# Kernel optimization log

Measured on AMD Instinct MI355X. Metric: run time of the kernel, lower is better.

Reference implementation:

```python
import jax, jax.numpy as jnp
import numpy as np

D = 20                 # input_dim
N = 1_000_000          # batch
NC = 2 ** (D + 1)      # number of dummy expert Linear(1,1) modules


def setup_inputs() -> dict:
    key = jax.random.key(0)
    ks = jax.random.split(key, 12)
    x = jax.random.randint(ks[0], (N, D), 0, 2).astype(jnp.float32)   # binary features
    t = jax.random.randint(ks[1], (N, 1), 0, 2).astype(jnp.float32)   # binary treatment
    y = jax.random.normal(ks[2], (N, 1), dtype=jnp.float32)           # outcome fed to dummy linears
    # Encoder dummy experts: one (w, b) pair per combination of (t, x)
    qz_w = jax.random.normal(ks[3], (NC,), dtype=jnp.float32) * 0.1
    qz_b = jax.random.normal(ks[4], (NC,), dtype=jnp.float32) * 0.1
    # Decoder per-feature Linear(1,1) for binary x
    dx_w = jax.random.normal(ks[5], (D,), dtype=jnp.float32) * 0.1
    dx_b = jax.random.normal(ks[6], (D,), dtype=jnp.float32) * 0.1
    # Decoder scalar Linear(1,1) heads
    t_w = jax.random.normal(ks[7], (), dtype=jnp.float32) * 0.1
    t_b = jnp.zeros((), jnp.float32)
    y0_w = jax.random.normal(ks[8], (), dtype=jnp.float32) * 0.1
    y0_b = jnp.zeros((), jnp.float32)
    y1_w = jax.random.normal(ks[9], (), dtype=jnp.float32) * 0.1
    y1_b = jnp.zeros((), jnp.float32)
    pz_logit = jnp.zeros((1,), jnp.float32)
    return {"x": x, "t": t, "y": y, "qz_w": qz_w, "qz_b": qz_b,
            "dx_w": dx_w, "dx_b": dx_b, "t_w": t_w, "t_b": t_b,
            "y0_w": y0_w, "y0_b": y0_b, "y1_w": y1_w, "y1_b": y1_b,
            "pz_logit": pz_logit}


def _combo_index(x, t):
    # itertools.product([0,1], repeat=D+1): combs[i][0] is the t bit (MSB),
    # combs[i][1:] are the x bits, so i = t*2^D + sum_j x_j * 2^(D-1-j).
    pow2 = (2 ** jnp.arange(D - 1, -1, -1)).astype(jnp.int32)   # [D]
    return t[:, 0].astype(jnp.int32) * (2 ** D) + x.astype(jnp.int32) @ pow2  # [N]


def _decode(z, t, dx_w, dx_b, t_w, t_b, y0_w, y0_b, y1_w, y1_b):
    # Vectorized form of per-feature Linear(1,1) loops: x_logits[:, i] = w_i*z + b_i
    x_logits = z * dx_w[None, :] + dx_b[None, :]          # [N, D]
    t_logits = z * t_w + t_b                              # [N, 1]
    y_logits = (z * y1_w + y1_b) * t + (z * y0_w + y0_b) * (1.0 - t)  # [N, 1]
    return x_logits, t_logits, y_logits


def reference(x, t, y, qz_w, qz_b, dx_w, dx_b, t_w, t_b,
              y0_w, y0_b, y1_w, y1_b, pz_logit):
    # Encoder (z_mode='binary'): sum over all 2^(D+1) experts of
    # (w_i*y + b_i) * onehot_mask_i == gather by combination index (inputs binary).
    idx = _combo_index(x, t)                                  # [N]
    z_logits = (qz_w[idx] * y[:, 0] + qz_b[idx])[:, None]     # [N, 1]
    n = x.shape[0]
    z0 = jnp.zeros((n, 1), jnp.float32)
    z1 = jnp.ones((n, 1), jnp.float32)
    x_logits0, t_logits0, y_logits0 = _decode(z0, t, dx_w, dx_b, t_w, t_b, y0_w, y0_b, y1_w, y1_b)
    x_logits1, t_logits1, y_logits1 = _decode(z1, t, dx_w, dx_b, t_w, t_b, y0_w, y0_b, y1_w, y1_b)
    return (z_logits, x_logits0, x_logits1, t_logits0, t_logits1,
            y_logits0, y_logits1, pz_logit)
```

## Files before the change

kernel.cpp:

```cpp
#include <hip/hip_runtime.h>

constexpr int D = 20;

typedef float f4 __attribute__((ext_vector_type(4)));
typedef unsigned int u32;

__device__ __forceinline__ u32 bf16_rne(float f) {
    u32 u = __float_as_uint(f);
    return (u + 0x7FFFu + ((u >> 16) & 1u)) >> 16;
}

__global__ __launch_bounds__(256) void cevae_build_tab(
    const f4* __restrict__ qw, const f4* __restrict__ qb,
    uint4* __restrict__ tab, int nq)
{
    int i = blockIdx.x * 256 + threadIdx.x;
    if (i >= nq) return;
    f4 w = qw[i];
    f4 b = qb[i];
    uint4 o;
    o.x = (bf16_rne(w.x) << 16) | bf16_rne(b.x);
    o.y = (bf16_rne(w.y) << 16) | bf16_rne(b.y);
    o.z = (bf16_rne(w.z) << 16) | bf16_rne(b.z);
    o.w = (bf16_rne(w.w) << 16) | bf16_rne(b.w);
    tab[i] = o;
}

__device__ __forceinline__ u32 combo_idx(const f4* xr, float tv) {
    f4 a = xr[0], b = xr[1], c = xr[2], d = xr[3], e = xr[4];
    u32 id = (tv != 0.0f) ? (1u << 20) : 0u;
    id |= ((u32)a.x) << 19; id |= ((u32)a.y) << 18;
    id |= ((u32)a.z) << 17; id |= ((u32)a.w) << 16;
    id |= ((u32)b.x) << 15; id |= ((u32)b.y) << 14;
    id |= ((u32)b.z) << 13; id |= ((u32)b.w) << 12;
    id |= ((u32)c.x) << 11; id |= ((u32)c.y) << 10;
    id |= ((u32)c.z) << 9;  id |= ((u32)c.w) << 8;
    id |= ((u32)d.x) << 7;  id |= ((u32)d.y) << 6;
    id |= ((u32)d.z) << 5;  id |= ((u32)d.w) << 4;
    id |= ((u32)e.x) << 3;  id |= ((u32)e.y) << 2;
    id |= ((u32)e.z) << 1;  id |= ((u32)e.w);
    return id;
}

template <bool USE_TAB>
__global__ __launch_bounds__(256) void cevae_fused8_kernel(
    const float* __restrict__ x, const float* __restrict__ t,
    const float* __restrict__ y, const u32* __restrict__ tab,
    const float* __restrict__ qz_w, const float* __restrict__ qz_b,
    const float* __restrict__ dx_w, const float* __restrict__ dx_b,
    const float* __restrict__ sc_tw, const float* __restrict__ sc_tb,
    const float* __restrict__ sc_y0w, const float* __restrict__ sc_y0b,
    const float* __restrict__ sc_y1w, const float* __restrict__ sc_y1b,
    const float* __restrict__ pz, float* __restrict__ out, int n_rows,
    int n_fill_blocks)
{
    int bid = blockIdx.x;
    int g = bid >> 3;
    size_t o3 = (size_t)n_rows * (size_t)(1 + 2 * D);

    if ((g & 3) == 0) {
        int sub = (g >> 2) * 8 + (bid & 7);
        int Qr = n_rows >> 2;
        int m = sub * 256 + threadIdx.x;
        if (m >= Qr) return;

        int n0 = m, n1 = m + Qr, n2 = m + 2 * Qr, n3 = m + 3 * Qr;

        float t0 = t[n0], t1 = t[n1], t2 = t[n2], t3 = t[n3];
        u32 i0 = combo_idx((const f4*)(x + (size_t)n0 * D), t0);
        u32 i1 = combo_idx((const f4*)(x + (size_t)n1 * D), t1);
        u32 i2 = combo_idx((const f4*)(x + (size_t)n2 * D), t2);
        u32 i3 = combo_idx((const f4*)(x + (size_t)n3 * D), t3);

        float y0v = y[n0], y1v = y[n1], y2v = y[n2], y3v = y[n3];

        float z0, z1, z2, z3;
        if (USE_TAB) {
            u32 g0 = tab[i0], g1 = tab[i1], g2 = tab[i2], g3 = tab[i3];
            z0 = fmaf(__uint_as_float(g0 & 0xFFFF0000u), y0v, __uint_as_float(g0 << 16));
            z1 = fmaf(__uint_as_float(g1 & 0xFFFF0000u), y1v, __uint_as_float(g1 << 16));
            z2 = fmaf(__uint_as_float(g2 & 0xFFFF0000u), y2v, __uint_as_float(g2 << 16));
            z3 = fmaf(__uint_as_float(g3 & 0xFFFF0000u), y3v, __uint_as_float(g3 << 16));
        } else {
            z0 = fmaf(qz_w[i0], y0v, qz_b[i0]);
            z1 = fmaf(qz_w[i1], y1v, qz_b[i1]);
            z2 = fmaf(qz_w[i2], y2v, qz_b[i2]);
            z3 = fmaf(qz_w[i3], y3v, qz_b[i3]);
        }
        out[n0] = z0;
        out[n1] = z1;
        out[n2] = z2;
        out[n3] = z3;

        float y0w = *sc_y0w, y0b = *sc_y0b;
        float y1w = *sc_y1w, y1b = *sc_y1b;
        float dy0 = y1b - y0b;
        float dy1 = (y1w + y1b) - (y0w + y0b), c1 = y0w + y0b;

        float* yl0 = out + o3 + 2 * (size_t)n_rows;
        float* yl1 = out + o3 + 3 * (size_t)n_rows;
        yl0[n0] = fmaf(t0, dy0, y0b);
        yl0[n1] = fmaf(t1, dy0, y0b);
        yl0[n2] = fmaf(t2, dy0, y0b);
        yl0[n3] = fmaf(t3, dy0, y0b);
        yl1[n0] = fmaf(t0, dy1, c1);
        yl1[n1] = fmaf(t1, dy1, c1);
        yl1[n2] = fmaf(t2, dy1, c1);
        yl1[n3] = fmaf(t3, dy1, c1);
        if (m == 0) out[o3 + 4 * (size_t)n_rows] = pz[0];
    } else {
        int fsub = (g - (g >> 2) - 1) * 8 + (bid & 7);
        unsigned Q = (unsigned)n_rows * D / 4;
        f4* r0 = (f4*)(out + n_rows);
        f4* r1 = r0 + Q;
        unsigned stride = (unsigned)n_fill_blocks * 256;
        unsigned q0 = (unsigned)fsub * 256 + threadIdx.x;
        for (unsigned q = q0; q < Q; q += stride) {
            int cb = (int)(q % 5u) * 4;
            float b0 = dx_b[cb + 0], b1 = dx_b[cb + 1];
            float b2 = dx_b[cb + 2], b3 = dx_b[cb + 3];
            float w0 = dx_w[cb + 0], w1 = dx_w[cb + 1];
            float w2 = dx_w[cb + 2], w3 = dx_w[cb + 3];
            f4 v0 = {b0, b1, b2, b3};
            f4 v1 = {w0 + b0, w1 + b1, w2 + b2, w3 + b3};
            __builtin_nontemporal_store(v0, r0 + q);
            __builtin_nontemporal_store(v1, r1 + q);
        }
        float tw = *sc_tw, tb = *sc_tb;
        f4 s0 = {tb, tb, tb, tb};
        float t1v = tw + tb;
        f4 s1 = {t1v, t1v, t1v, t1v};
        unsigned Qt = (unsigned)n_rows / 4;
        f4* h0 = (f4*)(out + o3);
        f4* h1 = (f4*)(out + o3 + (size_t)n_rows);
        for (unsigned q = q0; q < Qt; q += stride) {
            __builtin_nontemporal_store(s0, h0 + q);
            __builtin_nontemporal_store(s1, h1 + q);
        }
    }
}

extern "C" void kernel_launch(void* const* d_in, const int* in_sizes, int n_in,
                              void* d_out, int out_size, void* d_ws, size_t ws_size,
                              hipStream_t stream) {
    const float* x    = (const float*)d_in[0];
    const float* t    = (const float*)d_in[1];
    const float* y    = (const float*)d_in[2];
    const float* qz_w = (const float*)d_in[3];
    const float* qz_b = (const float*)d_in[4];
    const float* dx_w = (const float*)d_in[5];
    const float* dx_b = (const float*)d_in[6];
    const float* t_w  = (const float*)d_in[7];
    const float* t_b  = (const float*)d_in[8];
    const float* y0_w = (const float*)d_in[9];
    const float* y0_b = (const float*)d_in[10];
    const float* y1_w = (const float*)d_in[11];
    const float* y1_b = (const float*)d_in[12];
    const float* pz   = (const float*)d_in[13];
    float* out = (float*)d_out;

    int n_rows = in_sizes[0] / D;
    int nc     = in_sizes[3];

    int Qr = n_rows / 4;
    int n_rows_blocks = (Qr + 255) / 256;
    int n_rows_groups = (n_rows_blocks + 7) / 8;
    int n_groups = n_rows_groups * 4;
    int n_fill_blocks = (n_groups - n_rows_groups) * 8;

    size_t tab_bytes = (size_t)nc * sizeof(u32);
    if (ws_size >= tab_bytes) {
        uint4* tab = (uint4*)d_ws;
        int nq = nc / 4;
        cevae_build_tab<<<(nq + 255) / 256, 256, 0, stream>>>(
            (const f4*)qz_w, (const f4*)qz_b, tab, nq);
        cevae_fused8_kernel<true><<<n_groups * 8, 256, 0, stream>>>(
            x, t, y, (const u32*)tab, qz_w, qz_b, dx_w, dx_b, t_w, t_b,
            y0_w, y0_b, y1_w, y1_b, pz, out, n_rows, n_fill_blocks);
    } else {
        cevae_fused8_kernel<false><<<n_groups * 8, 256, 0, stream>>>(
            x, t, y, nullptr, qz_w, qz_b, dx_w, dx_b, t_w, t_b,
            y0_w, y0_b, y1_w, y1_b, pz, out, n_rows, n_fill_blocks);
    }
}
```

Before: 81.32 us.

## Fuse table build with constant fill and split row gather into separate kernel

The bf16 table build now shares one launch with the constant x/t logit fill, and the per-row gather (z, y logits) moves into its own kernel that runs afterwards. Before, the table build ran alone and the gather and fill blocks were interleaved in one launch. The goal is to hide the table build behind the large constant-fill writes. The row kernel also switches to nontemporal stores. In exchange the row gather becomes a separate dependent launch that cannot overlap with the fill.

```diff
diff --git a/kernel.cpp b/kernel.cpp
--- a/kernel.cpp
+++ b/kernel.cpp
@@ -10,23 +10,7 @@
     return (u + 0x7FFFu + ((u >> 16) & 1u)) >> 16;
 }
 
-__global__ __launch_bounds__(256) void cevae_build_tab(
-    const f4* __restrict__ qw, const f4* __restrict__ qb,
-    uint4* __restrict__ tab, int nq)
-{
-    int i = blockIdx.x * 256 + threadIdx.x;
-    if (i >= nq) return;
-    f4 w = qw[i];
-    f4 b = qb[i];
-    uint4 o;
-    o.x = (bf16_rne(w.x) << 16) | bf16_rne(b.x);
-    o.y = (bf16_rne(w.y) << 16) | bf16_rne(b.y);
-    o.z = (bf16_rne(w.z) << 16) | bf16_rne(b.z);
-    o.w = (bf16_rne(w.w) << 16) | bf16_rne(b.w);
-    tab[i] = o;
-}
-
-__device__ __forceinline__ u32 combo_idx(const f4* xr, float tv) {
+__device__ __forceinline__ u32 combo_idx(const f4* __restrict__ xr, float tv) {
     f4 a = xr[0], b = xr[1], c = xr[2], d = xr[3], e = xr[4];
     u32 id = (tv != 0.0f) ? (1u << 20) : 0u;
     id |= ((u32)a.x) << 19; id |= ((u32)a.y) << 18;
@@ -42,79 +26,33 @@
     return id;
 }
 
-template <bool USE_TAB>
-__global__ __launch_bounds__(256) void cevae_fused8_kernel(
-    const float* __restrict__ x, const float* __restrict__ t,
-    const float* __restrict__ y, const u32* __restrict__ tab,
-    const float* __restrict__ qz_w, const float* __restrict__ qz_b,
+__global__ __launch_bounds__(256) void cevae_A_build_fill(
+    const f4* __restrict__ qw, const f4* __restrict__ qb,
+    uint4* __restrict__ tab, int nq,
     const float* __restrict__ dx_w, const float* __restrict__ dx_b,
     const float* __restrict__ sc_tw, const float* __restrict__ sc_tb,
-    const float* __restrict__ sc_y0w, const float* __restrict__ sc_y0b,
-    const float* __restrict__ sc_y1w, const float* __restrict__ sc_y1b,
-    const float* __restrict__ pz, float* __restrict__ out, int n_rows,
-    int n_fill_blocks)
+    float* __restrict__ out, int n_rows,
+    int n_build_blocks, int n_fill_blocks)
 {
     int bid = blockIdx.x;
-    int g = bid >> 3;
-    size_t o3 = (size_t)n_rows * (size_t)(1 + 2 * D);
-
-    if ((g & 3) == 0) {
-        int sub = (g >> 2) * 8 + (bid & 7);
-        int Qr = n_rows >> 2;
-        int m = sub * 256 + threadIdx.x;
-        if (m >= Qr) return;
-
-        int n0 = m, n1 = m + Qr, n2 = m + 2 * Qr, n3 = m + 3 * Qr;
-
-        float t0 = t[n0], t1 = t[n1], t2 = t[n2], t3 = t[n3];
-        u32 i0 = combo_idx((const f4*)(x + (size_t)n0 * D), t0);
-        u32 i1 = combo_idx((const f4*)(x + (size_t)n1 * D), t1);
-        u32 i2 = combo_idx((const f4*)(x + (size_t)n2 * D), t2);
-        u32 i3 = combo_idx((const f4*)(x + (size_t)n3 * D), t3);
-
-        float y0v = y[n0], y1v = y[n1], y2v = y[n2], y3v = y[n3];
-
-        float z0, z1, z2, z3;
-        if (USE_TAB) {
-            u32 g0 = tab[i0], g1 = tab[i1], g2 = tab[i2], g3 = tab[i3];
-            z0 = fmaf(__uint_as_float(g0 & 0xFFFF0000u), y0v, __uint_as_float(g0 << 16));
-            z1 = fmaf(__uint_as_float(g1 & 0xFFFF0000u), y1v, __uint_as_float(g1 << 16));
-            z2 = fmaf(__uint_as_float(g2 & 0xFFFF0000u), y2v, __uint_as_float(g2 << 16));
-            z3 = fmaf(__uint_as_float(g3 & 0xFFFF0000u), y3v, __uint_as_float(g3 << 16));
-        } else {
-            z0 = fmaf(qz_w[i0], y0v, qz_b[i0]);
-            z1 = fmaf(qz_w[i1], y1v, qz_b[i1]);
-            z2 = fmaf(qz_w[i2], y2v, qz_b[i2]);
-            z3 = fmaf(qz_w[i3], y3v, qz_b[i3]);
-        }
-        out[n0] = z0;
-        out[n1] = z1;
-        out[n2] = z2;
-        out[n3] = z3;
-
-        float y0w = *sc_y0w, y0b = *sc_y0b;
-        float y1w = *sc_y1w, y1b = *sc_y1b;
-        float dy0 = y1b - y0b;
-        float dy1 = (y1w + y1b) - (y0w + y0b), c1 = y0w + y0b;
-
-        float* yl0 = out + o3 + 2 * (size_t)n_rows;
-        float* yl1 = out + o3 + 3 * (size_t)n_rows;
-        yl0[n0] = fmaf(t0, dy0, y0b);
-        yl0[n1] = fmaf(t1, dy0, y0b);
-        yl0[n2] = fmaf(t2, dy0, y0b);
-        yl0[n3] = fmaf(t3, dy0, y0b);
-        yl1[n0] = fmaf(t0, dy1, c1);
-        yl1[n1] = fmaf(t1, dy1, c1);
-        yl1[n2] = fmaf(t2, dy1, c1);
-        yl1[n3] = fmaf(t3, dy1, c1);
-        if (m == 0) out[o3 + 4 * (size_t)n_rows] = pz[0];
+    if (bid < n_build_blocks) {
+        int i = bid * 256 + threadIdx.x;
+        if (i >= nq) return;
+        f4 w = qw[i];
+        f4 b = qb[i];
+        uint4 o;
+        o.x = (bf16_rne(w.x) << 16) | bf16_rne(b.x);
+        o.y = (bf16_rne(w.y) << 16) | bf16_rne(b.y);
+        o.z = (bf16_rne(w.z) << 16) | bf16_rne(b.z);
+        o.w = (bf16_rne(w.w) << 16) | bf16_rne(b.w);
+        tab[i] = o;
     } else {
-        int fsub = (g - (g >> 2) - 1) * 8 + (bid & 7);
+        int fb = bid - n_build_blocks;
         unsigned Q = (unsigned)n_rows * D / 4;
         f4* r0 = (f4*)(out + n_rows);
         f4* r1 = r0 + Q;
         unsigned stride = (unsigned)n_fill_blocks * 256;
-        unsigned q0 = (unsigned)fsub * 256 + threadIdx.x;
+        unsigned q0 = (unsigned)fb * 256 + threadIdx.x;
         for (unsigned q = q0; q < Q; q += stride) {
             int cb = (int)(q % 5u) * 4;
             float b0 = dx_b[cb + 0], b1 = dx_b[cb + 1];
@@ -130,6 +68,7 @@
         f4 s0 = {tb, tb, tb, tb};
         float t1v = tw + tb;
         f4 s1 = {t1v, t1v, t1v, t1v};
+        size_t o3 = (size_t)n_rows * (size_t)(1 + 2 * D);
         unsigned Qt = (unsigned)n_rows / 4;
         f4* h0 = (f4*)(out + o3);
         f4* h1 = (f4*)(out + o3 + (size_t)n_rows);
@@ -138,6 +77,66 @@
             __builtin_nontemporal_store(s1, h1 + q);
         }
     }
+}
+
+template <bool USE_TAB>
+__global__ __launch_bounds__(256) void cevae_B_rows4(
+    const float* __restrict__ x, const float* __restrict__ t,
+    const float* __restrict__ y, const u32* __restrict__ tab,
+    const float* __restrict__ qz_w, const float* __restrict__ qz_b,
+    const float* __restrict__ sc_y0w, const float* __restrict__ sc_y0b,
+    const float* __restrict__ sc_y1w, const float* __restrict__ sc_y1b,
+    const float* __restrict__ pz, float* __restrict__ out, int n_rows)
+{
+    int Qr = n_rows >> 2;
+    int m = blockIdx.x * 256 + threadIdx.x;
+    if (m >= Qr) return;
+
+    int n0 = m, n1 = m + Qr, n2 = m + 2 * Qr, n3 = m + 3 * Qr;
+
+    float t0 = t[n0], t1 = t[n1], t2 = t[n2], t3 = t[n3];
+    u32 i0 = combo_idx((const f4*)(x + (size_t)n0 * D), t0);
+    u32 i1 = combo_idx((const f4*)(x + (size_t)n1 * D), t1);
+    u32 i2 = combo_idx((const f4*)(x + (size_t)n2 * D), t2);
+    u32 i3 = combo_idx((const f4*)(x + (size_t)n3 * D), t3);
+
+    float y0v = y[n0], y1v = y[n1], y2v = y[n2], y3v = y[n3];
+
+    float z0, z1, z2, z3;
+    if (USE_TAB) {
+        u32 g0 = tab[i0], g1 = tab[i1], g2 = tab[i2], g3 = tab[i3];
+        z0 = fmaf(__uint_as_float(g0 & 0xFFFF0000u), y0v, __uint_as_float(g0 << 16));
+        z1 = fmaf(__uint_as_float(g1 & 0xFFFF0000u), y1v, __uint_as_float(g1 << 16));
+        z2 = fmaf(__uint_as_float(g2 & 0xFFFF0000u), y2v, __uint_as_float(g2 << 16));
+        z3 = fmaf(__uint_as_float(g3 & 0xFFFF0000u), y3v, __uint_as_float(g3 << 16));
+    } else {
+        z0 = fmaf(qz_w[i0], y0v, qz_b[i0]);
+        z1 = fmaf(qz_w[i1], y1v, qz_b[i1]);
+        z2 = fmaf(qz_w[i2], y2v, qz_b[i2]);
+        z3 = fmaf(qz_w[i3], y3v, qz_b[i3]);
+    }
+    __builtin_nontemporal_store(z0, out + n0);
+    __builtin_nontemporal_store(z1, out + n1);
+    __builtin_nontemporal_store(z2, out + n2);
+    __builtin_nontemporal_store(z3, out + n3);
+
+    float y0w = *sc_y0w, y0b = *sc_y0b;
+    float y1w = *sc_y1w, y1b = *sc_y1b;
+    float dy0 = y1b - y0b;
+    float dy1 = (y1w + y1b) - (y0w + y0b), c1 = y0w + y0b;
+
+    size_t o3 = (size_t)n_rows * (size_t)(1 + 2 * D);
+    float* yl0 = out + o3 + 2 * (size_t)n_rows;
+    float* yl1 = out + o3 + 3 * (size_t)n_rows;
+    __builtin_nontemporal_store(fmaf(t0, dy0, y0b), yl0 + n0);
+    __builtin_nontemporal_store(fmaf(t1, dy0, y0b), yl0 + n1);
+    __builtin_nontemporal_store(fmaf(t2, dy0, y0b), yl0 + n2);
+    __builtin_nontemporal_store(fmaf(t3, dy0, y0b), yl0 + n3);
+    __builtin_nontemporal_store(fmaf(t0, dy1, c1), yl1 + n0);
+    __builtin_nontemporal_store(fmaf(t1, dy1, c1), yl1 + n1);
+    __builtin_nontemporal_store(fmaf(t2, dy1, c1), yl1 + n2);
+    __builtin_nontemporal_store(fmaf(t3, dy1, c1), yl1 + n3);
+    if (m == 0) out[o3 + 4 * (size_t)n_rows] = pz[0];
 }
 
 extern "C" void kernel_launch(void* const* d_in, const int* in_sizes, int n_in,
@@ -161,25 +160,28 @@
 
     int n_rows = in_sizes[0] / D;
     int nc     = in_sizes[3];
-
-    int Qr = n_rows / 4;
-    int n_rows_blocks = (Qr + 255) / 256;
-    int n_rows_groups = (n_rows_blocks + 7) / 8;
-    int n_groups = n_rows_groups * 4;
-    int n_fill_blocks = (n_groups - n_rows_groups) * 8;
+    int Qr     = n_rows / 4;
+    int n_b_blocks = (Qr + 255) / 256;
+    n_b_blocks = ((n_b_blocks + 7) / 8) * 8;
 
     size_t tab_bytes = (size_t)nc * sizeof(u32);
     if (ws_size >= tab_bytes) {
         uint4* tab = (uint4*)d_ws;
         int nq = nc / 4;
-        cevae_build_tab<<<(nq + 255) / 256, 256, 0, stream>>>(
-            (const f4*)qz_w, (const f4*)qz_b, tab, nq);
-        cevae_fused8_kernel<true><<<n_groups * 8, 256, 0, stream>>>(
-            x, t, y, (const u32*)tab, qz_w, qz_b, dx_w, dx_b, t_w, t_b,
-            y0_w, y0_b, y1_w, y1_b, pz, out, n_rows, n_fill_blocks);
+        int n_build_blocks = (nq + 255) / 256;
+        int n_fill_blocks  = 4096;
+        cevae_A_build_fill<<<n_build_blocks + n_fill_blocks, 256, 0, stream>>>(
+            (const f4*)qz_w, (const f4*)qz_b, tab, nq,
+            dx_w, dx_b, t_w, t_b, out, n_rows, n_build_blocks, n_fill_blocks);
+        cevae_B_rows4<true><<<n_b_blocks, 256, 0, stream>>>(
+            x, t, y, (const u32*)tab, qz_w, qz_b,
+            y0_w, y0_b, y1_w, y1_b, pz, out, n_rows);
     } else {
-        cevae_fused8_kernel<false><<<n_groups * 8, 256, 0, stream>>>(
-            x, t, y, nullptr, qz_w, qz_b, dx_w, dx_b, t_w, t_b,
-            y0_w, y0_b, y1_w, y1_b, pz, out, n_rows, n_fill_blocks);
+        cevae_A_build_fill<<<4096, 256, 0, stream>>>(
+            (const f4*)qz_w, (const f4*)qz_b, nullptr, 0,
+            dx_w, dx_b, t_w, t_b, out, n_rows, 0, 4096);
+        cevae_B_rows4<false><<<n_b_blocks, 256, 0, stream>>>(
+            x, t, y, nullptr, qz_w, qz_b,
+            y0_w, y0_b, y1_w, y1_b, pz, out, n_rows);
     }
 }
```

Result: faster. 68.51 us (-15.7%).
